# Kernel tuning notes

Measured on AMD Instinct MI355X. Metric: run time of the kernel, lower is better.

Reference implementation:

```python
import jax, jax.numpy as jnp
import numpy as np

D_STATE = 64
D_CONV = 5
HEADDIM = 64
EXPAND = 2


def setup_inputs() -> dict:
    key = jax.random.key(0)
    ks = jax.random.split(key, 12)
    b, ch, h, w = 4, 128, 64, 64
    d_inner = EXPAND * ch
    nheads = d_inner // HEADDIM
    conv_ch = d_inner + 2 * D_STATE
    d_in_proj = 2 * d_inner + 2 * D_STATE + nheads
    s = lambda k, shape, scale: jax.random.normal(k, shape, jnp.float32) * scale
    return {
        "noisy": s(ks[0], (b, ch, h, w), 1.0),
        "aux": s(ks[1], (b, ch, h, w), 1.0),
        "ln_gamma": jnp.ones((ch,), jnp.float32),
        "ln_beta": jnp.zeros((ch,), jnp.float32),
        "in_proj_w": s(ks[2], (d_in_proj, ch), ch ** -0.5),
        "conv_w": s(ks[3], (conv_ch, D_CONV), D_CONV ** -0.5),
        "conv_b": s(ks[4], (conv_ch,), 0.02),
        "A_log": jnp.log(jnp.linspace(1.0, 16.0, nheads)).astype(jnp.float32),
        "dt_bias": s(ks[5], (nheads,), 0.1),
        "D": jnp.ones((nheads,), jnp.float32),
        "rms_w": jnp.ones((d_inner,), jnp.float32),
        "out_proj_w": s(ks[6], (ch, d_inner), d_inner ** -0.5),
        "ff_w1": s(ks[7], (ch, ch, 3, 3), (ch * 9) ** -0.5),
        "ff_b1": jnp.zeros((ch,), jnp.float32),
        "ff_w2": s(ks[8], (ch, ch, 3, 3), (ch * 9) ** -0.5),
        "ff_b2": jnp.zeros((ch,), jnp.float32),
    }


def _mamba2(u, in_proj_w, conv_w, conv_b, A_log, dt_bias, D_skip, rms_w, out_proj_w):
    # u: (b, L, d_model). Mamba2 with ngroups=1, headdim=64.
    b, L, d = u.shape
    d_inner = EXPAND * d
    nheads = d_inner // HEADDIM
    zxbcdt = u @ in_proj_w.T  # (b, L, 2*d_inner + 2*d_state + nheads)
    z = zxbcdt[..., :d_inner]
    xBC = zxbcdt[..., d_inner:2 * d_inner + 2 * D_STATE]
    dt = jax.nn.softplus(zxbcdt[..., -nheads:] + dt_bias)  # (b, L, h)
    # causal depthwise conv1d along L + SiLU
    xBC_c = jnp.transpose(xBC, (0, 2, 1))  # (b, C, L)
    xBC_c = jax.lax.conv_general_dilated(
        xBC_c, conv_w[:, None, :], (1,), [(D_CONV - 1, 0)],
        feature_group_count=xBC_c.shape[1])
    xBC = jax.nn.silu(jnp.transpose(xBC_c + conv_b[None, :, None], (0, 2, 1)))
    x = xBC[..., :d_inner]
    B = xBC[..., d_inner:d_inner + D_STATE]  # (b, L, n)
    C = xBC[..., d_inner + D_STATE:]         # (b, L, n)
    A = -jnp.exp(A_log)                      # (h,)
    xh = x.reshape(b, L, nheads, HEADDIM)    # (b, L, h, p)
    dA = jnp.exp(dt * A)                     # (b, L, h)

    def step(hstate, inputs):
        dA_t, dt_t, x_t, B_t, C_t = inputs
        hstate = hstate * dA_t[:, :, None, None] + jnp.einsum('bh,bhp,bn->bhpn', dt_t, x_t, B_t)
        y_t = jnp.einsum('bhpn,bn->bhp', hstate, C_t)
        return hstate, y_t

    init = jnp.zeros((b, nheads, HEADDIM, D_STATE), u.dtype)
    xs = (jnp.moveaxis(dA, 1, 0), jnp.moveaxis(dt, 1, 0), jnp.moveaxis(xh, 1, 0),
          jnp.moveaxis(B, 1, 0), jnp.moveaxis(C, 1, 0))
    _, ys = jax.lax.scan(step, init, xs)
    y = jnp.moveaxis(ys, 0, 1) + xh * D_skip[None, None, :, None]  # (b, L, h, p)
    y = y.reshape(b, L, d_inner)
    # gated RMSNorm: rmsnorm(y * silu(z)) * weight
    y = y * jax.nn.silu(z)
    y = y * jax.lax.rsqrt(jnp.mean(y * y, axis=-1, keepdims=True) + 1e-5) * rms_w
    return y @ out_proj_w.T


def _conv3x3_reflect(x, w, b):
    x = jnp.pad(x, ((0, 0), (0, 0), (1, 1), (1, 1)), mode='reflect')
    return jax.lax.conv_general_dilated(x, w, (1, 1), 'VALID') + b[None, :, None, None]


def reference(noisy, aux, ln_gamma, ln_beta, in_proj_w, conv_w, conv_b, A_log,
              dt_bias, D, rms_w, out_proj_w, ff_w1, ff_b1, ff_w2, ff_b2):
    b, c, h, w = noisy.shape
    flat = jnp.transpose(noisy, (0, 2, 3, 1)).reshape(b, h * w, c)
    mu = jnp.mean(flat, axis=-1, keepdims=True)
    var = jnp.var(flat, axis=-1, keepdims=True)
    normed = (flat - mu) * jax.lax.rsqrt(var + 1e-5) * ln_gamma + ln_beta
    m = _mamba2(normed, in_proj_w, conv_w, conv_b, A_log, dt_bias, D, rms_w, out_proj_w)
    m = jnp.transpose(m.reshape(b, h, w, c), (0, 3, 1, 2))
    y = noisy + m
    ff = jax.nn.relu(_conv3x3_reflect(y, ff_w1, ff_b1))
    ff = jax.nn.relu(_conv3x3_reflect(ff, ff_w2, ff_b2))
    y = y + ff
    return (y, aux)
```

## Files before the change

### kernel.cpp

```cpp
#include <hip/hip_runtime.h>
#include <cstddef>

#define B_      4
#define C_      128
#define L_      4096
#define DIN     256
#define NH      4
#define HD      64
#define DS      64
#define CONVCH  384
#define DPROJ   644
#define CHUNK   64
#define NCHUNK  64

typedef short bf16x8 __attribute__((ext_vector_type(8)));
typedef float floatx16 __attribute__((ext_vector_type(16)));

__device__ __forceinline__ float siluf(float v) { return v / (1.f + __expf(-v)); }

__device__ __forceinline__ ushort f2bf(float v) {
  unsigned u = __float_as_uint(v);
  unsigned r = (u + 0x7fff + ((u >> 16) & 1)) >> 16;
  return (ushort)r;
}
__device__ __forceinline__ float bf2f(ushort h) {
  return __uint_as_float((unsigned)h << 16);
}

__device__ __forceinline__ void split8(float4 v0, float4 v1, bf16x8& hi, bf16x8& lo) {
  float f[8] = {v0.x, v0.y, v0.z, v0.w, v1.x, v1.y, v1.z, v1.w};
#pragma unroll
  for (int j = 0; j < 8; ++j) {
    ushort h = f2bf(f[j]);
    hi[j] = (short)h;
    lo[j] = (short)f2bf(f[j] - bf2f(h));
  }
}

__global__ __launch_bounds__(256) void wprep_all(
    const float* __restrict__ ipw, ushort* __restrict__ Bh, ushort* __restrict__ Bl,
    const float* __restrict__ opw, ushort* __restrict__ Oh, ushort* __restrict__ Ol,
    const float* __restrict__ fw1, ushort* __restrict__ Wt1,
    const float* __restrict__ fw2, ushort* __restrict__ Wt2) {
  int bi = blockIdx.x;
  int t = threadIdx.x;
  if (bi < 176) {
    int e = bi * 256 + t;
    int d = e >> 6;
    int c0 = (e & 63) * 2;
    int kk = c0 >> 4;
    int l = (d & 31) + 32 * ((c0 & 15) >> 3);
    int j = c0 & 7;
    size_t off = (((size_t)(d >> 5)) * 8 + kk) * 512 + l * 8 + j;
    float v0 = d < 644 ? ipw[(size_t)d * 128 + c0] : 0.f;
    float v1 = d < 644 ? ipw[(size_t)d * 128 + c0 + 1] : 0.f;
    ushort h0 = f2bf(v0), h1 = f2bf(v1);
    *(unsigned*)(Bh + off) = (unsigned)h0 | ((unsigned)h1 << 16);
    *(unsigned*)(Bl + off) = (unsigned)f2bf(v0 - bf2f(h0)) |
                             ((unsigned)f2bf(v1 - bf2f(h1)) << 16);
  } else if (bi < 304) {
    int e = (bi - 176) * 256 + t;
    int d = e >> 8;
    int c = e & 255;
    size_t f = ((size_t)(d >> 5) * 16 + (c >> 4)) * 512 +
               ((d & 31) + 32 * ((c & 15) >> 3)) * 8 + (c & 7);
    float v = opw[(size_t)d * 256 + c];
    ushort h = f2bf(v);
    Oh[f] = h;
    Ol[f] = f2bf(v - bf2f(h));
  } else {
    const float* fw = bi < 432 ? fw1 : fw2;
    ushort* Wt = bi < 432 ? Wt1 : Wt2;
    int co = (bi - 304) & 127;
    int cb = co >> 5;
    for (int e = t; e < 1152; e += 256) {
      int tap = e >> 7;
      int ci = e & 127;
      int kk = ci >> 4, k16 = ci & 15;
      int l = (co & 31) + 32 * (k16 >> 3);
      int off = ((tap * 8 + kk) * 4 + cb) * 512 + l * 8 + (k16 & 7);
      Wt[off] = f2bf(fw[(size_t)co * 1152 + ci * 9 + tap]);
    }
  }
}

__global__ __launch_bounds__(512) void ln_gemm1(
    const float* __restrict__ noisy, const float* __restrict__ gamma,
    const float* __restrict__ beta,
    const ushort* __restrict__ Bh, const ushort* __restrict__ Bl,
    float* __restrict__ ZX) {
  int row = blockIdx.x, b = blockIdx.y;
  int t = threadIdx.x;
  __shared__ float tile[32 * 129];
  __shared__ float ps[16][32], pq[16][32];
  __shared__ float smu[32], srs[32];
  __shared__ __align__(16) ushort AhL[4096];
  __shared__ __align__(16) ushort AlL[4096];
  int px = t & 31, cg = t >> 5;
  float s = 0.f, s2 = 0.f;
  const float* src = noisy + ((size_t)b * C_) * L_ + row * 32;
  for (int i = 0; i < 8; ++i) {
    int c = cg * 8 + i;
    float v = src[(size_t)c * L_ + px];
    tile[px * 129 + c] = v;
    s += v; s2 += v * v;
  }
  ps[cg][px] = s; pq[cg][px] = s2;
  __syncthreads();
  if (t < 32) {
    float a = 0.f, qq = 0.f;
#pragma unroll
    for (int g = 0; g < 16; ++g) { a += ps[g][t]; qq += pq[g][t]; }
    float mu = a * (1.f / 128.f);
    float var = qq * (1.f / 128.f) - mu * mu;
    smu[t] = mu;
    srs[t] = rsqrtf(var + 1e-5f);
  }
  __syncthreads();
  for (int idx = t; idx < 2048; idx += 512) {
    int p2 = idx >> 6;
    int c0 = (idx & 63) * 2;
    float v0 = (tile[p2 * 129 + c0] - smu[p2]) * srs[p2] * gamma[c0] + beta[c0];
    float v1 = (tile[p2 * 129 + c0 + 1] - smu[p2]) * srs[p2] * gamma[c0 + 1] + beta[c0 + 1];
    int kk = c0 >> 4;
    int l = p2 + 32 * ((c0 & 15) >> 3);
    int j = c0 & 7;
    int off = kk * 512 + l * 8 + j;
    ushort h0 = f2bf(v0), h1 = f2bf(v1);
    *(unsigned*)(AhL + off) = (unsigned)h0 | ((unsigned)h1 << 16);
    *(unsigned*)(AlL + off) = (unsigned)f2bf(v0 - bf2f(h0)) |
                              ((unsigned)f2bf(v1 - bf2f(h1)) << 16);
  }
  __syncthreads();
  int wv = t >> 6, lane = t & 63;
  int db = wv & 1, bq = wv >> 1;
  int rowadd = 4 * (lane >> 5);
  for (int bn = bq; bn < 11; bn += 4) {
    floatx16 acc;
#pragma unroll
    for (int i = 0; i < 16; ++i) acc[i] = 0.f;
    size_t bbase = ((size_t)(bn * 2 + db) * 8) * 64 + lane;
    const bf16x8* pBh = (const bf16x8*)Bh + bbase;
    const bf16x8* pBl = (const bf16x8*)Bl + bbase;
#pragma unroll
    for (int kk = 0; kk < 8; ++kk) {
      bf16x8 ah = *(const bf16x8*)(AhL + kk * 512 + lane * 8);
      bf16x8 al = *(const bf16x8*)(AlL + kk * 512 + lane * 8);
      bf16x8 bh = pBh[kk * 64];
      bf16x8 bl = pBl[kk * 64];
      acc = __builtin_amdgcn_mfma_f32_32x32x16_bf16(ah, bh, acc, 0, 0, 0);
      acc = __builtin_amdgcn_mfma_f32_32x32x16_bf16(al, bh, acc, 0, 0, 0);
      acc = __builtin_amdgcn_mfma_f32_32x32x16_bf16(ah, bl, acc, 0, 0, 0);
    }
    int d = bn * 64 + db * 32 + (lane & 31);
    if (d < 644) {
#pragma unroll
      for (int r = 0; r < 16; ++r) {
        int rowm = (r & 3) + 8 * (r >> 2) + rowadd;
        int pix = row * 32 + rowm;
        ZX[((size_t)(b * L_ + pix)) * DPROJ + d] = acc[r];
      }
    }
  }
}

__global__ __launch_bounds__(384) void conv1d_silu(
    const float* __restrict__ ZX, const float* __restrict__ cw,
    const float* __restrict__ cb, float* __restrict__ XBC) {
  int ch = threadIdx.x;
  int l0 = blockIdx.x * 16, b = blockIdx.y;
  const float* base = ZX + ((size_t)b * L_) * DPROJ + DIN + ch;
  float w0 = cw[ch * 5], w1 = cw[ch * 5 + 1], w2 = cw[ch * 5 + 2],
        w3 = cw[ch * 5 + 3], w4 = cw[ch * 5 + 4];
  float bias = cb[ch];
  float win[20];
#pragma unroll
  for (int i = 0; i < 20; ++i) {
    int ll = l0 - 4 + i;
    win[i] = ll >= 0 ? base[(size_t)ll * DPROJ] : 0.f;
  }
  float* dst = XBC + ((size_t)(b * L_ + l0)) * CONVCH + ch;
#pragma unroll
  for (int j = 0; j < 16; ++j) {
    float acc = bias + w0 * win[j] + w1 * win[j + 1] + w2 * win[j + 2] +
                w3 * win[j + 3] + w4 * win[j + 4];
    dst[(size_t)j * CONVCH] = siluf(acc);
  }
}

#define UPDA(k, B4, C4) \
  st[4*k+0] = st[4*k+0]*da + cf*B4.x; y0 += st[4*k+0]*C4.x; \
  st[4*k+1] = st[4*k+1]*da + cf*B4.y; y1 += st[4*k+1]*C4.y; \
  st[4*k+2] = st[4*k+2]*da + cf*B4.z; y2 += st[4*k+2]*C4.z; \
  st[4*k+3] = st[4*k+3]*da + cf*B4.w; y3 += st[4*k+3]*C4.w;

__global__ __launch_bounds__(256, 4) void scan_passA(
    const float* __restrict__ XBC, const float* __restrict__ ZX,
    const float* __restrict__ dt_bias, const float* __restrict__ A_log,
    float* __restrict__ YL, float* __restrict__ SC, float* __restrict__ PC,
    float* __restrict__ CUM) {
  int chunk = blockIdx.x, h = blockIdx.y, b = blockIdx.z;
  int t = threadIdx.x;
  int p = t >> 2, q = t & 3;
  int bh = b * NH + h;
  __shared__ float sdt[CHUNK], sda[CHUNK];
  __shared__ float sB[32][64];
  __shared__ float sCc[32][64];
  __shared__ float sx[32][64];
  if (t < CHUNK) {
    int l = chunk * CHUNK + t;
    float v = ZX[((size_t)(b * L_ + l)) * DPROJ + 640 + h] + dt_bias[h];
    float dt = v > 20.f ? v : log1pf(expf(v));
    sdt[t] = dt;
    sda[t] = expf(dt * -expf(A_log[h]));
  }
  size_t rowbase = ((size_t)b * L_ + (size_t)chunk * CHUNK) * CONVCH;
  float* __restrict__ yl = YL + ((size_t)b * L_ + (size_t)chunk * CHUNK) * DIN + h * HD + p;
  float* __restrict__ cumout = CUM + (size_t)bh * L_ + chunk * CHUNK;
  float st[16];
#pragma unroll
  for (int j = 0; j < 16; ++j) st[j] = 0.f;
  float cum = 1.f;
  for (int half = 0; half < 2; ++half) {
    __syncthreads();
#pragma unroll
    for (int i = 0; i < 2; ++i) {
      int e = t + i * 256;
      int row = e >> 4, c4 = (e & 15) * 4;
      const float* gsrc = XBC + rowbase + (size_t)(half * 32 + row) * CONVCH;
      *(float4*)&sB[row][c4]  = *(const float4*)(gsrc + DIN + c4);
      *(float4*)&sCc[row][c4] = *(const float4*)(gsrc + DIN + DS + c4);
      *(float4*)&sx[row][c4]  = *(const float4*)(gsrc + h * HD + c4);
    }
    __syncthreads();
#pragma unroll 4
    for (int tl = 0; tl < 32; ++tl) {
      int tg = half * 32 + tl;
      float da = sda[tg], dtv = sdt[tg];
      float x = sx[tl][p];
      float cf = dtv * x;
      const float4* br = (const float4*)&sB[tl][q * 16];
      const float4* cr = (const float4*)&sCc[tl][q * 16];
      float4 B0 = br[0], B1 = br[1], B2 = br[2], B3 = br[3];
      float4 C0 = cr[0], C1 = cr[1], C2 = cr[2], C3 = cr[3];
      float y0 = 0.f, y1 = 0.f, y2 = 0.f, y3 = 0.f;
      UPDA(0, B0, C0) UPDA(1, B1, C1) UPDA(2, B2, C2) UPDA(3, B3, C3)
      float y = (y0 + y1) + (y2 + y3);
      y += __shfl_xor(y, 1);
      y += __shfl_xor(y, 2);
      cum *= da;
      if (q == 0) yl[(size_t)tg * DIN] = y;
      if (t == 0) cumout[tg] = cum;
    }
  }
  float* scp = SC + ((size_t)bh * NCHUNK + chunk) * 4096 + p * 64 + q * 16;
  *(float4*)(scp + 0)  = make_float4(st[0], st[1], st[2], st[3]);
  *(float4*)(scp + 4)  = make_float4(st[4], st[5], st[6], st[7]);
  *(float4*)(scp + 8)  = make_float4(st[8], st[9], st[10], st[11]);
  *(float4*)(scp + 12) = make_float4(st[12], st[13], st[14], st[15]);
  if (t == 0) PC[bh * NCHUNK + chunk] = cum;
}

__global__ __launch_bounds__(256) void scan_passB(
    float* __restrict__ SC, const float* __restrict__ PC) {
  int bh = blockIdx.x >> 4;
  int eg = blockIdx.x & 15;
  int e = eg * 256 + threadIdx.x;
  float h = 0.f;
#pragma unroll 8
  for (int c = 0; c < NCHUNK; ++c) {
    size_t idx = ((size_t)bh * NCHUNK + c) * 4096 + e;
    float s = SC[idx];
    float pcv = PC[bh * NCHUNK + c];
    SC[idx] = h;
    h = h * pcv + s;
  }
}

__global__ __launch_bounds__(512) void passC_gate(
    const float* __restrict__ XBC, const float* __restrict__ SC,
    const float* __restrict__ CUM, const float* __restrict__ Dp,
    const float* __restrict__ YL, const float* __restrict__ ZX,
    const float* __restrict__ rmsw,
    const ushort* __restrict__ Oh, const ushort* __restrict__ Ol,
    const float* __restrict__ noisy, float* __restrict__ YRES) {
  __shared__ float yt[8192];
  __shared__ __align__(16) ushort fr[16384];
  int hc = blockIdx.x, b = blockIdx.y;
  int chunk = hc >> 1;
  int l0 = hc * 32;
  int t = threadIdx.x;
  int wv = t >> 6, lane = t & 63;
  size_t pix0g = (size_t)b * L_ + l0;
  float* sCcf  = (float*)fr;
  float* scumf = sCcf + 2048;

  float4 zr[4];
  {
    int lp = t & 31, slot2 = t >> 5;
#pragma unroll
    for (int it = 0; it < 2; ++it) {
      const float* z = ZX + (pix0g + it * 16 + slot2) * DPROJ;
      zr[it * 2]     = *(const float4*)(z + lp * 4);
      zr[it * 2 + 1] = *(const float4*)(z + 128 + lp * 4);
    }
  }
  for (int i = t; i < 2048; i += 512) {
    *(float4*)&yt[i * 4] = *(const float4*)&YL[pix0g * DIN + (size_t)i * 4];
  }
  {
    int px = t >> 4, slot = t & 15;
    float4 cv = *(const float4*)(XBC + (pix0g + px) * CONVCH + DIN + DS + slot * 4);
    ((float4*)sCcf)[px * 16 + (slot ^ (px & 7))] = cv;
    if (t < 128) {
      int hh = t >> 5, px2 = t & 31;
      scumf[t] = CUM[((size_t)(b * NH + hh)) * L_ + l0 + px2];
    }
  }
  __syncthreads();

  {
    int px = t >> 4, c4 = (t & 15) * 4;
    const float* xs = XBC + (pix0g + px) * CONVCH;
#pragma unroll
    for (int hh = 0; hh < 4; ++hh) {
      float4 xv = *(const float4*)(xs + hh * HD + c4);
      float dv = Dp[hh];
      float* dst = &yt[px * 256 + hh * 64 + c4];
      dst[0] += xv.x * dv; dst[1] += xv.y * dv;
      dst[2] += xv.z * dv; dst[3] += xv.w * dv;
    }
  }
  __syncthreads();

  {
    int h1 = wv >> 1, ptile = wv & 1;
    int arow = lane & 31;
    const float* Sb = SC + (((size_t)(b * NH + h1)) * NCHUNK + chunk) * 4096 +
                      (size_t)(ptile * 32 + (lane & 31)) * 64 + (lane >> 5) * 8;
    const float4* av = (const float4*)sCcf + arow * 16;
    int s0 = (lane >> 5) * 2;
    floatx16 acc;
#pragma unroll
    for (int i = 0; i < 16; ++i) acc[i] = 0.f;
#pragma unroll
    for (int kk = 0; kk < 4; ++kk) {
      float4 b0 = *(const float4*)(Sb + kk * 16);
      float4 b1 = *(const float4*)(Sb + kk * 16 + 4);
      int sa = kk * 4 + s0;
      float4 a0 = av[sa ^ (arow & 7)];
      float4 a1 = av[(sa + 1) ^ (arow & 7)];
      bf16x8 ah, al, bh, bl;
      split8(a0, a1, ah, al);
      split8(b0, b1, bh, bl);
      acc = __builtin_amdgcn_mfma_f32_32x32x16_bf16(ah, bh, acc, 0, 0, 0);
      acc = __builtin_amdgcn_mfma_f32_32x32x16_bf16(al, bh, acc, 0, 0, 0);
      acc = __builtin_amdgcn_mfma_f32_32x32x16_bf16(ah, bl, acc, 0, 0, 0);
    }
    int col = h1 * 64 + ptile * 32 + (lane & 31);
    int radd = 4 * (lane >> 5);
#pragma unroll
    for (int r = 0; r < 16; ++r) {
      int px = (r & 3) + 8 * (r >> 2) + radd;
      yt[px * 256 + col] += acc[r] * scumf[h1 * 32 + px];
    }
  }
  __syncthreads();

  ushort* AhL = fr;
  ushort* AlL = fr + 8192;
  {
    int lp = t & 31;
    int slot = t >> 5;
    float4 w0 = *(const float4*)(rmsw + lp * 4);
    float4 w1 = *(const float4*)(rmsw + 128 + lp * 4);
#pragma unroll
    for (int it = 0; it < 2; ++it) {
      int pl = it * 16 + slot;
      const float* y = &yt[pl * 256];
      float4 y0 = *(const float4*)(y + lp * 4);
      float4 y1 = *(const float4*)(y + 128 + lp * 4);
      float4 z0 = zr[it * 2];
      float4 z1 = zr[it * 2 + 1];
      float g[8];
      g[0] = y0.x * siluf(z0.x); g[1] = y0.y * siluf(z0.y);
      g[2] = y0.z * siluf(z0.z); g[3] = y0.w * siluf(z0.w);
      g[4] = y1.x * siluf(z1.x); g[5] = y1.y * siluf(z1.y);
      g[6] = y1.z * siluf(z1.z); g[7] = y1.w * siluf(z1.w);
      float ss = 0.f;
#pragma unroll
      for (int j = 0; j < 8; ++j) ss += g[j] * g[j];
      ss += __shfl_xor(ss, 16);
      ss += __shfl_xor(ss, 8);
      ss += __shfl_xor(ss, 4);
      ss += __shfl_xor(ss, 2);
      ss += __shfl_xor(ss, 1);
      float rs = rsqrtf(ss * (1.f / 256.f) + 1e-5f);
      float o[8];
      o[0] = g[0] * rs * w0.x; o[1] = g[1] * rs * w0.y;
      o[2] = g[2] * rs * w0.z; o[3] = g[3] * rs * w0.w;
      o[4] = g[4] * rs * w1.x; o[5] = g[5] * rs * w1.y;
      o[6] = g[6] * rs * w1.z; o[7] = g[7] * rs * w1.w;
#pragma unroll
      for (int grp = 0; grp < 2; ++grp) {
        int d = grp * 128 + lp * 4;
        int off = (d >> 4) * 512 + (pl + 32 * ((d & 15) >> 3)) * 8 + (d & 7);
        ushort h0 = f2bf(o[grp*4+0]), h1 = f2bf(o[grp*4+1]);
        ushort h2 = f2bf(o[grp*4+2]), h3 = f2bf(o[grp*4+3]);
        uint2 hv, lv;
        hv.x = (unsigned)h0 | ((unsigned)h1 << 16);
        hv.y = (unsigned)h2 | ((unsigned)h3 << 16);
        lv.x = (unsigned)f2bf(o[grp*4+0] - bf2f(h0)) | ((unsigned)f2bf(o[grp*4+1] - bf2f(h1)) << 16);
        lv.y = (unsigned)f2bf(o[grp*4+2] - bf2f(h2)) | ((unsigned)f2bf(o[grp*4+3] - bf2f(h3)) << 16);
        *(uint2*)(AhL + off) = hv;
        *(uint2*)(AlL + off) = lv;
      }
    }
  }
  __syncthreads();

  floatx16 acc;
#pragma unroll
  for (int i = 0; i < 16; ++i) acc[i] = 0.f;
  int bn = wv >> 1, db = wv & 1;
  int rowadd = 4 * (lane >> 5);
  if (wv < 4) {
    const bf16x8* pBh = (const bf16x8*)Oh;
    const bf16x8* pBl = (const bf16x8*)Ol;
    size_t bbase = ((size_t)(bn * 2 + db) * 16) * 64 + lane;
#pragma unroll
    for (int kk = 0; kk < 16; ++kk) {
      bf16x8 ah = *(const bf16x8*)(AhL + kk * 512 + lane * 8);
      bf16x8 al = *(const bf16x8*)(AlL + kk * 512 + lane * 8);
      bf16x8 bh = pBh[bbase + (size_t)kk * 64];
      bf16x8 bl = pBl[bbase + (size_t)kk * 64];
      acc = __builtin_amdgcn_mfma_f32_32x32x16_bf16(ah, bh, acc, 0, 0, 0);
      acc = __builtin_amdgcn_mfma_f32_32x32x16_bf16(al, bh, acc, 0, 0, 0);
      acc = __builtin_amdgcn_mfma_f32_32x32x16_bf16(ah, bl, acc, 0, 0, 0);
    }
  }
  __syncthreads();

  float* tile = (float*)fr;
  if (wv < 4) {
#pragma unroll
    for (int r = 0; r < 16; ++r) {
      int rowp = (r & 3) + 8 * (r >> 2) + rowadd;
      int col = bn * 64 + db * 32 + (lane & 31);
      tile[rowp * 129 + col] = acc[r];
    }
  }
  __syncthreads();
  for (int idx = t; idx < 4096; idx += 512) {
    int c = idx >> 5, px = idx & 31;
    size_t o = ((size_t)(b * C_ + c)) * L_ + l0 + px;
    YRES[o] = noisy[o] + tile[px * 129 + c];
  }
}

template <int MODE>
__global__ __launch_bounds__(512) void conv3x3_direct(
    const void* __restrict__ inv, const ushort* __restrict__ Wt,
    const float* __restrict__ bias, const float* __restrict__ res,
    void* __restrict__ outv, const float* __restrict__ aux) {
  int y = blockIdx.x, b = blockIdx.y;
  int t = threadIdx.x;
  if (MODE == 1 && blockIdx.z == 1) {
    const float4* s = (const float4*)aux;
    float4* d = (float4*)((float*)outv + 2097152);
    int base = (b * 64 + y) * 512 + t;
#pragma unroll
    for (int k = 0; k < 4; ++k) d[base + k * 131072] = s[base + k * 131072];
    return;
  }
  __shared__ __align__(16) ushort lds[3 * 64 * 128];
  int lane = t & 63;
  int wv = t >> 6;
  int ry[3];
  ry[0] = y == 0 ? 1 : y - 1;
  ry[1] = y;
  ry[2] = y == 63 ? 62 : y + 1;
  {
    int x = lane;
    for (int u = wv; u < 48; u += 8) {
      int r = u / 16;
      int cib = u % 16;
      int ci0 = cib * 8;
      ushort vals[8];
#pragma unroll
      for (int j = 0; j < 8; ++j) {
        size_t src = ((size_t)(b * C_ + ci0 + j)) * L_ + ry[r] * 64 + x;
        if (MODE == 0) vals[j] = f2bf(((const float*)inv)[src]);
        else           vals[j] = ((const ushort*)inv)[src];
      }
      int idx = (r * 64 + x) * 128 + (cib ^ (x & 15)) * 8;
      *(int4*)&lds[idx] = *(int4*)vals;
    }
  }
  __syncthreads();
  int cb = wv >> 1, nb = wv & 1;
  int n = lane & 31, hi = lane >> 5;
  floatx16 acc0, acc1;
#pragma unroll
  for (int i = 0; i < 16; ++i) { acc0[i] = 0.f; acc1[i] = 0.f; }
  const bf16x8* pW = (const bf16x8*)Wt;
  for (int tap = 0; tap < 9; ++tap) {
    int ky = tap / 3, kx = tap % 3;
    int xg = nb * 32 + n + kx - 1;
    int xx = xg < 0 ? 1 : (xg > 63 ? 62 : xg);
    int base = (ky * 64 + xx) * 128;
    int xs = xx & 15;
#pragma unroll
    for (int kk = 0; kk < 8; ++kk) {
      bf16x8 av = pW[(size_t)((tap * 8 + kk) * 4 + cb) * 64 + lane];
      bf16x8 bv = *(const bf16x8*)&lds[base + ((kk * 2 + hi) ^ xs) * 8];
      if (kk & 1) acc1 = __builtin_amdgcn_mfma_f32_32x32x16_bf16(av, bv, acc1, 0, 0, 0);
      else        acc0 = __builtin_amdgcn_mfma_f32_32x32x16_bf16(av, bv, acc0, 0, 0, 0);
    }
  }
  int x0 = nb * 32 + (lane & 31);
  int rowadd = 4 * (lane >> 5);
#pragma unroll
  for (int r = 0; r < 16; ++r) {
    int rowm = (r & 3) + 8 * (r >> 2) + rowadd;
    int co = cb * 32 + rowm;
    size_t o = ((size_t)(b * C_ + co)) * L_ + y * 64 + x0;
    float v = fmaxf(acc0[r] + acc1[r] + bias[co], 0.f);
    if (MODE == 0) {
      ((ushort*)outv)[o] = f2bf(v);
    } else {
      ((float*)outv)[o] = v + res[o];
    }
  }
}

extern "C" void kernel_launch(void* const* d_in, const int* in_sizes, int n_in,
                              void* d_out, int out_size, void* d_ws, size_t ws_size,
                              hipStream_t stream) {
  const float* noisy   = (const float*)d_in[0];
  const float* aux     = (const float*)d_in[1];
  const float* ln_g    = (const float*)d_in[2];
  const float* ln_b    = (const float*)d_in[3];
  const float* ipw     = (const float*)d_in[4];
  const float* cw      = (const float*)d_in[5];
  const float* cbv     = (const float*)d_in[6];
  const float* A_log   = (const float*)d_in[7];
  const float* dt_bias = (const float*)d_in[8];
  const float* Dp      = (const float*)d_in[9];
  const float* rmsw    = (const float*)d_in[10];
  const float* opw     = (const float*)d_in[11];
  const float* fw1     = (const float*)d_in[12];
  const float* fb1     = (const float*)d_in[13];
  const float* fw2     = (const float*)d_in[14];
  const float* fb2     = (const float*)d_in[15];
  float* out = (float*)d_out;
  float* ws  = (float*)d_ws;

  const size_t OFF_ZX   = 0;
  const size_t OFF_XBC  = OFF_ZX + 16384UL * 644;
  const size_t OFF_SCN  = OFF_XBC + 16384UL * 384;
  const size_t OFF_WT   = OFF_SCN + 4194304UL;
  const size_t OFF_WO   = OFF_WT + 73728UL;
  const size_t OFF_CUM  = OFF_WT + 131072UL;
  const size_t OFF_YL   = OFF_CUM + 65536UL;
  const size_t OFF_PC   = OFF_YL + 16384UL * 256;
  const size_t OFF_WT2  = OFF_PC + 1024UL;
  const size_t OFF_YRES = OFF_WT2 + 73728UL;

  float* ZX   = ws + OFF_ZX;
  float* XBC  = ws + OFF_XBC;
  float* SC   = ws + OFF_SCN;
  float* CUM  = ws + OFF_CUM;
  float* YL   = ws + OFF_YL;
  float* PC   = ws + OFF_PC;
  ushort* Bnh  = (ushort*)(ws + OFF_YL);
  ushort* Bnl  = Bnh + 45056UL * 2;
  ushort* Wt1 = (ushort*)(ws + OFF_WT);
  ushort* Woh  = (ushort*)(ws + OFF_WO);
  ushort* Wol  = Woh + 32768UL;
  ushort* Wt2 = (ushort*)(ws + OFF_WT2);
  ushort* FF1 = (ushort*)(ws + OFF_SCN);
  float* YRES = ws + OFF_YRES;

  wprep_all<<<560, 256, 0, stream>>>(ipw, Bnh, Bnl, opw, Woh, Wol, fw1, Wt1, fw2, Wt2);
  ln_gemm1<<<dim3(128, 4), 512, 0, stream>>>(noisy, ln_g, ln_b, Bnh, Bnl, ZX);
  conv1d_silu<<<dim3(L_ / 16, B_), 384, 0, stream>>>(ZX, cw, cbv, XBC);
  scan_passA<<<dim3(NCHUNK, NH, B_), 256, 0, stream>>>(XBC, ZX, dt_bias, A_log, YL, SC, PC, CUM);
  scan_passB<<<256, 256, 0, stream>>>(SC, PC);
  passC_gate<<<dim3(NCHUNK * 2, B_), 512, 0, stream>>>(XBC, SC, CUM, Dp, YL, ZX,
                                                       rmsw, Woh, Wol, noisy, YRES);
  conv3x3_direct<0><<<dim3(64, 4), 512, 0, stream>>>(YRES, Wt1, fb1, nullptr, FF1, nullptr);
  conv3x3_direct<1><<<dim3(64, 4, 2), 512, 0, stream>>>(FF1, Wt2, fb2, YRES, out, aux);
}
```

Measured before the change: 238.9 us.

## Rewrite intra-chunk SSM scan as chunked matmuls on MFMA with split-bf16

The intra-chunk scan in scan_passA is replaced by the SSD quadratic formulation. The kernel computes C·Bᵀ, applies a causal decay mask from a wave-level prefix sum of dt, multiplies by X to get the local outputs, and forms the chunk-end state as a weighted Xᵀ·B. All three products use bf16 MFMA with a hi/lo split (three MFMAs per tile) to approximate fp32 accuracy. This removes the serial 64-step per-timestep recurrence in exchange for more FLOPs, larger shared-memory tiles and some precision loss from the bf16x3 split.

```diff
diff --git a/kernel.cpp b/kernel.cpp
--- a/kernel.cpp
+++ b/kernel.cpp
@@ -188,77 +188,155 @@
   }
 }
 
-#define UPDA(k, B4, C4) \
-  st[4*k+0] = st[4*k+0]*da + cf*B4.x; y0 += st[4*k+0]*C4.x; \
-  st[4*k+1] = st[4*k+1]*da + cf*B4.y; y1 += st[4*k+1]*C4.y; \
-  st[4*k+2] = st[4*k+2]*da + cf*B4.z; y2 += st[4*k+2]*C4.z; \
-  st[4*k+3] = st[4*k+3]*da + cf*B4.w; y3 += st[4*k+3]*C4.w;
-
-__global__ __launch_bounds__(256, 4) void scan_passA(
+__global__ __launch_bounds__(256) void scan_passA(
     const float* __restrict__ XBC, const float* __restrict__ ZX,
     const float* __restrict__ dt_bias, const float* __restrict__ A_log,
     float* __restrict__ YL, float* __restrict__ SC, float* __restrict__ PC,
     float* __restrict__ CUM) {
   int chunk = blockIdx.x, h = blockIdx.y, b = blockIdx.z;
   int t = threadIdx.x;
-  int p = t >> 2, q = t & 3;
+  int wv = t >> 6, lane = t & 63;
   int bh = b * NH + h;
-  __shared__ float sdt[CHUNK], sda[CHUNK];
-  __shared__ float sB[32][64];
-  __shared__ float sCc[32][64];
-  __shared__ float sx[32][64];
-  if (t < CHUNK) {
-    int l = chunk * CHUNK + t;
-    float v = ZX[((size_t)(b * L_ + l)) * DPROJ + 640 + h] + dt_bias[h];
+  int l0 = chunk * CHUNK;
+  size_t pix0g = (size_t)b * L_ + l0;
+  __shared__ float sB[64 * 68];
+  __shared__ float sC[64 * 68];
+  __shared__ float sXT[64 * 68];
+  __shared__ float sdt[64], sla[64], sw[64];
+
+#pragma unroll
+  for (int i = 0; i < 12; ++i) {
+    int e = t + i * 256;
+    int reg = e >> 10;
+    int idx2 = e & 1023;
+    int row = idx2 >> 4, c4 = (idx2 & 15) * 4;
+    const float* gsrc = XBC + (pix0g + row) * CONVCH;
+    if (reg == 0) {
+      *(float4*)&sB[row * 68 + c4] = *(const float4*)(gsrc + DIN + c4);
+    } else if (reg == 1) {
+      *(float4*)&sC[row * 68 + c4] = *(const float4*)(gsrc + DIN + DS + c4);
+    } else {
+      float4 xv = *(const float4*)(gsrc + h * HD + c4);
+      sXT[(c4 + 0) * 68 + row] = xv.x;
+      sXT[(c4 + 1) * 68 + row] = xv.y;
+      sXT[(c4 + 2) * 68 + row] = xv.z;
+      sXT[(c4 + 3) * 68 + row] = xv.w;
+    }
+  }
+  if (wv == 0) {
+    float v = ZX[(pix0g + lane) * DPROJ + 640 + h] + dt_bias[h];
     float dt = v > 20.f ? v : log1pf(expf(v));
-    sdt[t] = dt;
-    sda[t] = expf(dt * -expf(A_log[h]));
-  }
-  size_t rowbase = ((size_t)b * L_ + (size_t)chunk * CHUNK) * CONVCH;
-  float* __restrict__ yl = YL + ((size_t)b * L_ + (size_t)chunk * CHUNK) * DIN + h * HD + p;
-  float* __restrict__ cumout = CUM + (size_t)bh * L_ + chunk * CHUNK;
-  float st[16];
-#pragma unroll
-  for (int j = 0; j < 16; ++j) st[j] = 0.f;
-  float cum = 1.f;
-  for (int half = 0; half < 2; ++half) {
-    __syncthreads();
-#pragma unroll
-    for (int i = 0; i < 2; ++i) {
-      int e = t + i * 256;
-      int row = e >> 4, c4 = (e & 15) * 4;
-      const float* gsrc = XBC + rowbase + (size_t)(half * 32 + row) * CONVCH;
-      *(float4*)&sB[row][c4]  = *(const float4*)(gsrc + DIN + c4);
-      *(float4*)&sCc[row][c4] = *(const float4*)(gsrc + DIN + DS + c4);
-      *(float4*)&sx[row][c4]  = *(const float4*)(gsrc + h * HD + c4);
-    }
-    __syncthreads();
-#pragma unroll 4
-    for (int tl = 0; tl < 32; ++tl) {
-      int tg = half * 32 + tl;
-      float da = sda[tg], dtv = sdt[tg];
-      float x = sx[tl][p];
-      float cf = dtv * x;
-      const float4* br = (const float4*)&sB[tl][q * 16];
-      const float4* cr = (const float4*)&sCc[tl][q * 16];
-      float4 B0 = br[0], B1 = br[1], B2 = br[2], B3 = br[3];
-      float4 C0 = cr[0], C1 = cr[1], C2 = cr[2], C3 = cr[3];
-      float y0 = 0.f, y1 = 0.f, y2 = 0.f, y3 = 0.f;
-      UPDA(0, B0, C0) UPDA(1, B1, C1) UPDA(2, B2, C2) UPDA(3, B3, C3)
-      float y = (y0 + y1) + (y2 + y3);
-      y += __shfl_xor(y, 1);
-      y += __shfl_xor(y, 2);
-      cum *= da;
-      if (q == 0) yl[(size_t)tg * DIN] = y;
-      if (t == 0) cumout[tg] = cum;
-    }
-  }
-  float* scp = SC + ((size_t)bh * NCHUNK + chunk) * 4096 + p * 64 + q * 16;
-  *(float4*)(scp + 0)  = make_float4(st[0], st[1], st[2], st[3]);
-  *(float4*)(scp + 4)  = make_float4(st[4], st[5], st[6], st[7]);
-  *(float4*)(scp + 8)  = make_float4(st[8], st[9], st[10], st[11]);
-  *(float4*)(scp + 12) = make_float4(st[12], st[13], st[14], st[15]);
-  if (t == 0) PC[bh * NCHUNK + chunk] = cum;
+    float A = -expf(A_log[h]);
+    float cdt = dt;
+#pragma unroll
+    for (int off = 1; off < 64; off <<= 1) {
+      float u = __shfl_up(cdt, off);
+      if (lane >= off) cdt += u;
+    }
+    float la = cdt * A;
+    float la63 = __shfl(la, 63);
+    float cum = expf(la);
+    sdt[lane] = dt;
+    sla[lane] = la;
+    sw[lane] = expf(la63 - la) * dt;
+    CUM[(size_t)bh * L_ + l0 + lane] = cum;
+    if (lane == 63) PC[bh * NCHUNK + chunk] = cum;
+  }
+  __syncthreads();
+
+  int l31 = lane & 31, lhi = lane >> 5;
+  int rowadd = 4 * lhi;
+  int ttile = wv >> 1, stile = wv & 1;
+
+  floatx16 acc;
+#pragma unroll
+  for (int i = 0; i < 16; ++i) acc[i] = 0.f;
+#pragma unroll
+  for (int kb = 0; kb < 4; ++kb) {
+    const float* ap = &sC[(ttile * 32 + l31) * 68 + kb * 16 + lhi * 8];
+    const float* bp = &sB[(stile * 32 + l31) * 68 + kb * 16 + lhi * 8];
+    float4 a0 = *(const float4*)ap, a1 = *(const float4*)(ap + 4);
+    float4 b0 = *(const float4*)bp, b1 = *(const float4*)(bp + 4);
+    bf16x8 ah, al, bh, bl;
+    split8(a0, a1, ah, al);
+    split8(b0, b1, bh, bl);
+    acc = __builtin_amdgcn_mfma_f32_32x32x16_bf16(ah, bh, acc, 0, 0, 0);
+    acc = __builtin_amdgcn_mfma_f32_32x32x16_bf16(al, bh, acc, 0, 0, 0);
+    acc = __builtin_amdgcn_mfma_f32_32x32x16_bf16(ah, bl, acc, 0, 0, 0);
+  }
+  __syncthreads();
+
+  float* sG = sC;
+#pragma unroll
+  for (int r = 0; r < 16; ++r) {
+    int tt = ttile * 32 + (r & 3) + 8 * (r >> 2) + rowadd;
+    int ss = stile * 32 + l31;
+    float val = 0.f;
+    if (ss <= tt) val = acc[r] * __expf(sla[tt] - sla[ss]) * sdt[ss];
+    sG[tt * 68 + ss] = val;
+  }
+  __syncthreads();
+
+  {
+    int ptile = stile;
+    floatx16 acc2;
+#pragma unroll
+    for (int i = 0; i < 16; ++i) acc2[i] = 0.f;
+#pragma unroll
+    for (int kb = 0; kb < 4; ++kb) {
+      const float* ap = &sG[(ttile * 32 + l31) * 68 + kb * 16 + lhi * 8];
+      const float* bp = &sXT[(ptile * 32 + l31) * 68 + kb * 16 + lhi * 8];
+      float4 a0 = *(const float4*)ap, a1 = *(const float4*)(ap + 4);
+      float4 b0 = *(const float4*)bp, b1 = *(const float4*)(bp + 4);
+      bf16x8 ah, al, bh, bl;
+      split8(a0, a1, ah, al);
+      split8(b0, b1, bh, bl);
+      acc2 = __builtin_amdgcn_mfma_f32_32x32x16_bf16(ah, bh, acc2, 0, 0, 0);
+      acc2 = __builtin_amdgcn_mfma_f32_32x32x16_bf16(al, bh, acc2, 0, 0, 0);
+      acc2 = __builtin_amdgcn_mfma_f32_32x32x16_bf16(ah, bl, acc2, 0, 0, 0);
+    }
+#pragma unroll
+    for (int r = 0; r < 16; ++r) {
+      int tt = ttile * 32 + (r & 3) + 8 * (r >> 2) + rowadd;
+      int p = ptile * 32 + l31;
+      YL[(pix0g + tt) * DIN + h * HD + p] = acc2[r];
+    }
+  }
+
+  {
+    int p2tile = wv >> 1, ntile = wv & 1;
+    floatx16 acc3;
+#pragma unroll
+    for (int i = 0; i < 16; ++i) acc3[i] = 0.f;
+#pragma unroll
+    for (int kb = 0; kb < 4; ++kb) {
+      int s0 = kb * 16 + lhi * 8;
+      const float* ap = &sXT[(p2tile * 32 + l31) * 68 + s0];
+      float4 a0 = *(const float4*)ap, a1 = *(const float4*)(ap + 4);
+      float4 w0 = *(const float4*)&sw[s0], w1 = *(const float4*)&sw[s0 + 4];
+      a0.x *= w0.x; a0.y *= w0.y; a0.z *= w0.z; a0.w *= w0.w;
+      a1.x *= w1.x; a1.y *= w1.y; a1.z *= w1.z; a1.w *= w1.w;
+      int n = ntile * 32 + l31;
+      float bf[8];
+#pragma unroll
+      for (int j = 0; j < 8; ++j) bf[j] = sB[(s0 + j) * 68 + n];
+      float4 b0 = make_float4(bf[0], bf[1], bf[2], bf[3]);
+      float4 b1 = make_float4(bf[4], bf[5], bf[6], bf[7]);
+      bf16x8 ah, al, bh, bl;
+      split8(a0, a1, ah, al);
+      split8(b0, b1, bh, bl);
+      acc3 = __builtin_amdgcn_mfma_f32_32x32x16_bf16(ah, bh, acc3, 0, 0, 0);
+      acc3 = __builtin_amdgcn_mfma_f32_32x32x16_bf16(al, bh, acc3, 0, 0, 0);
+      acc3 = __builtin_amdgcn_mfma_f32_32x32x16_bf16(ah, bl, acc3, 0, 0, 0);
+    }
+    float* scp = SC + ((size_t)bh * NCHUNK + chunk) * 4096;
+#pragma unroll
+    for (int r = 0; r < 16; ++r) {
+      int p = p2tile * 32 + (r & 3) + 8 * (r >> 2) + rowadd;
+      int n = ntile * 32 + l31;
+      scp[p * 64 + n] = acc3[r];
+    }
+  }
 }
 
 __global__ __launch_bounds__(256) void scan_passB(
```

Result: faster. 225.1 us (-5.8%).
